# Optimization experiments

Hardware: AMD Instinct MI355X
Metric: run time of the kernel (lower is better)

The kernel has to match this reference:

```python
import jax, jax.numpy as jnp
import numpy as np

B, W, C_BLK, N_EMBD, N_HEADS = 512, 128, 24, 32, 2


def setup_inputs() -> dict:
    key = jax.random.key(0)
    k1, k2, k3, k4 = jax.random.split(key, 4)
    x = jax.random.normal(k1, (B, W, C_BLK, N_EMBD), dtype=jnp.float32)
    x_end_idx = jax.random.randint(k2, (B, W), 0, C_BLK, dtype=jnp.int32)
    # nn.Linear(n_embd, 3*n_embd, bias=False): store transposed so y = x @ w
    w_attn = jax.random.normal(k3, (N_EMBD, 3 * N_EMBD), dtype=jnp.float32) * (1.0 / np.sqrt(N_EMBD))
    w_proj = jax.random.normal(k4, (N_EMBD, N_EMBD), dtype=jnp.float32) * (1.0 / np.sqrt(N_EMBD))
    return {"x": x, "x_end_idx": x_end_idx, "w_attn": w_attn, "w_proj": w_proj}


def reference(x, x_end_idx, w_attn, w_proj):
    # x: [B, W, c, C]; causal self-attention over the char axis c, per (batch, word).
    Bd, Wd, c, C = x.shape
    H = N_HEADS
    D = C // H
    qkv = x @ w_attn                               # [B, W, c, 3C]
    q, k, v = jnp.split(qkv, 3, axis=-1)
    # [B, W, H, c, D]
    q = q.reshape(Bd, Wd, c, H, D).transpose(0, 1, 3, 2, 4)
    k = k.reshape(Bd, Wd, c, H, D).transpose(0, 1, 3, 2, 4)
    v = v.reshape(Bd, Wd, c, H, D).transpose(0, 1, 3, 2, 4)
    scale = 1.0 / jnp.sqrt(jnp.asarray(D, dtype=x.dtype))
    scores = jnp.einsum('bwhqd,bwhkd->bwhqk', q, k) * scale   # [B, W, H, c, c]
    causal = jnp.tril(jnp.ones((c, c), dtype=bool))
    scores = jnp.where(causal, scores, jnp.asarray(-jnp.inf, dtype=scores.dtype))
    att = jax.nn.softmax(scores, axis=-1)
    out = jnp.einsum('bwhqk,bwhkd->bwhqd', att, v)            # [B, W, H, c, D]
    out = out.transpose(0, 1, 3, 2, 4).reshape(Bd, Wd, c, C)
    out = out @ w_proj                                        # c_proj (dropout in eval mode = identity)
    out = x + out                                             # residual
    # Vectorized last-token gather: pick out[b, w, x_end_idx[b, w], :]
    idx = x_end_idx[:, :, None, None].astype(jnp.int32)       # [B, W, 1, 1]
    samples = jnp.take_along_axis(out, jnp.broadcast_to(idx, (Bd, Wd, 1, C)), axis=2)
    return samples.squeeze(2)                                 # [B, W, C]
```

## Files before the change

### kernel.cpp

```cpp
#include <hip/hip_runtime.h>


#define CB      24
#define CC      32
#define DD      16
#define THREEC  96
#define NBW     (512 * 128)
#define WPB     4
#define XSS     34

__device__ __align__(16) float4 g_M4[2][8][CC];
__device__ __align__(16) float4 g_P4[2][8][CC];

__global__ void precompute_mp(const float* __restrict__ w_attn,
                              const float* __restrict__ w_proj)
{
    const int idx = blockIdx.x * 256 + threadIdx.x;
    const int h = idx >> 8, e4 = (idx >> 5) & 7, c = idx & 31;
    float m[4], p[4];
    #pragma unroll
    for (int k = 0; k < 4; ++k) {
        const int e = 4 * e4 + k;
        float mm = 0.f, pp = 0.f;
        #pragma unroll
        for (int d = 0; d < DD; ++d) {
            const int i = DD * h + d;
            mm = fmaf(w_attn[e * THREEC + i],          w_attn[c * THREEC + CC + i], mm);
            pp = fmaf(w_attn[e * THREEC + 2 * CC + i], w_proj[i * CC + c],          pp);
        }
        m[k] = 0.25f * mm;
        p[k] = pp;
    }
    g_M4[h][e4][c] = make_float4(m[0], m[1], m[2], m[3]);
    g_P4[h][e4][c] = make_float4(p[0], p[1], p[2], p[3]);
}

struct __align__(16) WaveSmem {
    float xs[CB][XSS];
    float rks[2][CC];
    float ps[2][CC];
    float ys[2][CC];
};

__device__ __forceinline__ void wave_fence() {
    __asm__ volatile("s_waitcnt lgkmcnt(0)" ::: "memory");
}

__global__ __launch_bounds__(256, 8) void char_attn_kernel(
    const float* __restrict__ x,
    const int*   __restrict__ xend,
    float*       __restrict__ out)
{
    __shared__ WaveSmem sm[WPB];

    const int tid  = threadIdx.x;
    const int lane = tid & 63;
    const int wave = tid >> 6;
    WaveSmem& S = sm[wave];

    const int i32  = lane & 31;
    const int half = lane >> 5;

    const int sbid = __builtin_amdgcn_readfirstlane(blockIdx.x * WPB + wave);
    const int sq   = __builtin_amdgcn_readfirstlane(xend[sbid]);
    const int L    = sq + 1;

    const float* __restrict__ xb = x + (size_t)sbid * (CB * CC);
    const float* __restrict__ xq = xb + sq * CC;

    {
        const float2* xb2 = (const float2*)xb;
        const int n2 = L * (CC / 2);
        for (int t = lane; t < n2; t += 64) {
            float2 v = xb2[t];
            const int r = t >> 4, c = (t & 15) * 2;
            *(float2*)&S.xs[r][c] = v;
        }
    }

    {
        float a0 = 0.f, a1 = 0.f, a2 = 0.f, a3 = 0.f;
        #pragma unroll
        for (int e4 = 0; e4 < 8; ++e4) {
            const float4 mv = g_M4[half][e4][i32];
            const float4 xv = *(const float4*)(xq + e4 * 4);
            a0 = fmaf(mv.x, xv.x, a0);
            a1 = fmaf(mv.y, xv.y, a1);
            a2 = fmaf(mv.z, xv.z, a2);
            a3 = fmaf(mv.w, xv.w, a3);
        }
        S.rks[half][i32] = (a0 + a1) + (a2 + a3);
    }
    wave_fence();

    {
        float sc = -INFINITY;
        if (i32 <= sq) {
            const float4* rk4 = (const float4*)&S.rks[half][0];
            float a0 = 0.f, a1 = 0.f, a2 = 0.f, a3 = 0.f;
            #pragma unroll
            for (int e4 = 0; e4 < 8; ++e4) {
                const float4 rv = rk4[e4];
                const float2 x0 = *(const float2*)&S.xs[i32][e4 * 4];
                const float2 x1 = *(const float2*)&S.xs[i32][e4 * 4 + 2];
                a0 = fmaf(rv.x, x0.x, a0);
                a1 = fmaf(rv.y, x0.y, a1);
                a2 = fmaf(rv.z, x1.x, a2);
                a3 = fmaf(rv.w, x1.y, a3);
            }
            sc = (a0 + a1) + (a2 + a3);
        }
        float m = sc;
        #pragma unroll
        for (int off = 16; off >= 1; off >>= 1)
            m = fmaxf(m, __shfl_xor(m, off));
        const float e = (i32 <= sq) ? __expf(sc - m) : 0.f;
        float sum = e;
        #pragma unroll
        for (int off = 16; off >= 1; off >>= 1)
            sum += __shfl_xor(sum, off);
        S.ps[half][i32] = __fdividef(e, sum);
    }
    wave_fence();

    {
        float a0 = 0.f, a1 = 0.f;
        int j = 0;
        for (; j + 1 < L; j += 2) {
            const float2 p2 = *(const float2*)&S.ps[half][j];
            a0 = fmaf(p2.x, S.xs[j][i32],     a0);
            a1 = fmaf(p2.y, S.xs[j + 1][i32], a1);
        }
        if (j < L)
            a0 = fmaf(S.ps[half][j], S.xs[j][i32], a0);
        S.ys[half][i32] = a0 + a1;
    }
    wave_fence();

    {
        const float4* y4 = (const float4*)&S.ys[half][0];
        float a0 = 0.f, a1 = 0.f, a2 = 0.f, a3 = 0.f;
        #pragma unroll
        for (int e4 = 0; e4 < 8; ++e4) {
            const float4 pv = g_P4[half][e4][i32];
            const float4 yv = y4[e4];
            a0 = fmaf(pv.x, yv.x, a0);
            a1 = fmaf(pv.y, yv.y, a1);
            a2 = fmaf(pv.z, yv.z, a2);
            a3 = fmaf(pv.w, yv.w, a3);
        }
        float t = (a0 + a1) + (a2 + a3);
        t += __shfl_xor(t, 32);
        if (lane < CC)
            out[(size_t)sbid * CC + i32] = t + S.xs[sq][i32];
    }
}

extern "C" void kernel_launch(void* const* d_in, const int* in_sizes, int n_in,
                              void* d_out, int out_size, void* d_ws, size_t ws_size,
                              hipStream_t stream) {
    const float* x      = (const float*)d_in[0];
    const int*   xend   = (const int*)d_in[1];
    const float* w_attn = (const float*)d_in[2];
    const float* w_proj = (const float*)d_in[3];
    float* out = (float*)d_out;

    precompute_mp<<<dim3(2), dim3(256), 0, stream>>>(w_attn, w_proj);
    char_attn_kernel<<<dim3(NBW / WPB), dim3(WPB * 64), 0, stream>>>(
        x, xend, out);
}
```

Measured before the change: 294.6 us.

## Process 16 samples per wave with register prefetch of next sample

Each wave now loops over 16 (batch,word) pairs instead of one. The M and P weight fragments are held in registers across the loop, and the next sample's x rows are prefetched into registers while the current one is computed. The softmax drops the max subtraction and folds the normalization into the y output. This amortizes weight loads and hides global load latency, at the cost of more registers and lower occupancy (launch bounds drop from 8 to 4), fewer blocks, and a risk of exp overflow with no max shift.

```diff
diff --git a/kernel.cpp b/kernel.cpp
--- a/kernel.cpp
+++ b/kernel.cpp
@@ -7,6 +7,8 @@
 #define THREEC  96
 #define NBW     (512 * 128)
 #define WPB     4
+#define NPW     16
+#define NBLK    (NBW / (WPB * NPW))
 #define XSS     34
 
 __device__ __align__(16) float4 g_M4[2][8][CC];
@@ -46,7 +48,7 @@
     __asm__ volatile("s_waitcnt lgkmcnt(0)" ::: "memory");
 }
 
-__global__ __launch_bounds__(256, 8) void char_attn_kernel(
+__global__ __launch_bounds__(256, 4) void char_attn_kernel(
     const float* __restrict__ x,
     const int*   __restrict__ xend,
     float*       __restrict__ out)
@@ -61,98 +63,138 @@
     const int i32  = lane & 31;
     const int half = lane >> 5;
 
-    const int sbid = __builtin_amdgcn_readfirstlane(blockIdx.x * WPB + wave);
-    const int sq   = __builtin_amdgcn_readfirstlane(xend[sbid]);
-    const int L    = sq + 1;
-
-    const float* __restrict__ xb = x + (size_t)sbid * (CB * CC);
-    const float* __restrict__ xq = xb + sq * CC;
-
+    const int sbase = __builtin_amdgcn_readfirstlane(
+                          (blockIdx.x * WPB + wave) * NPW);
+    const int* __restrict__ xe = xend + sbase;
+
+    float4 Mw[8], Pw[8];
+    #pragma unroll
+    for (int e4 = 0; e4 < 8; ++e4) {
+        Mw[e4] = g_M4[half][e4][i32];
+        Pw[e4] = g_P4[half][e4][i32];
+    }
+
+    int sq  = __builtin_amdgcn_readfirstlane(xe[0]);
+    int sqn = __builtin_amdgcn_readfirstlane(xe[1]);
+    float2 pf[6];
+    #pragma unroll
+    for (int i = 0; i < 6; ++i) pf[i] = make_float2(0.f, 0.f);
     {
-        const float2* xb2 = (const float2*)xb;
-        const int n2 = L * (CC / 2);
-        for (int t = lane; t < n2; t += 64) {
-            float2 v = xb2[t];
-            const int r = t >> 4, c = (t & 15) * 2;
-            *(float2*)&S.xs[r][c] = v;
-        }
-    }
-
-    {
-        float a0 = 0.f, a1 = 0.f, a2 = 0.f, a3 = 0.f;
+        const float2* xp = (const float2*)(x + (size_t)sbase * (CB * CC));
+        const int n2 = (sq + 1) * (CC / 2);
         #pragma unroll
-        for (int e4 = 0; e4 < 8; ++e4) {
-            const float4 mv = g_M4[half][e4][i32];
-            const float4 xv = *(const float4*)(xq + e4 * 4);
-            a0 = fmaf(mv.x, xv.x, a0);
-            a1 = fmaf(mv.y, xv.y, a1);
-            a2 = fmaf(mv.z, xv.z, a2);
-            a3 = fmaf(mv.w, xv.w, a3);
-        }
-        S.rks[half][i32] = (a0 + a1) + (a2 + a3);
-    }
-    wave_fence();
-
-    {
-        float sc = -INFINITY;
-        if (i32 <= sq) {
-            const float4* rk4 = (const float4*)&S.rks[half][0];
+        for (int i = 0; i < 6; ++i) {
+            const int t = lane + 64 * i;
+            if (t < n2) pf[i] = xp[t];
+        }
+    }
+
+    for (int k = 0; k < NPW; ++k) {
+        const int pid = sbase + k;
+        const float* __restrict__ xb = x + (size_t)pid * (CB * CC);
+        const float* __restrict__ xq = xb + sq * CC;
+
+        float4 xqv[8];
+        #pragma unroll
+        for (int e = 0; e < 8; ++e) xqv[e] = *(const float4*)(xq + 4 * e);
+
+        {
+            const int n2 = (sq + 1) * (CC / 2);
+            #pragma unroll
+            for (int i = 0; i < 6; ++i) {
+                const int t = lane + 64 * i;
+                if (t < n2) {
+                    const int r = t >> 4, c = (t & 15) * 2;
+                    *(float2*)&S.xs[r][c] = pf[i];
+                }
+            }
+        }
+
+        if (k + 1 < NPW) {
+            const float2* xp = (const float2*)(x + (size_t)(pid + 1) * (CB * CC));
+            const int n2n = (sqn + 1) * (CC / 2);
+            #pragma unroll
+            for (int i = 0; i < 6; ++i) {
+                const int t = lane + 64 * i;
+                if (t < n2n) pf[i] = xp[t];
+            }
+        }
+        const int sqf = __builtin_amdgcn_readfirstlane(
+                            xe[(k + 2 < NPW) ? k + 2 : NPW - 1]);
+
+        {
             float a0 = 0.f, a1 = 0.f, a2 = 0.f, a3 = 0.f;
             #pragma unroll
             for (int e4 = 0; e4 < 8; ++e4) {
-                const float4 rv = rk4[e4];
-                const float2 x0 = *(const float2*)&S.xs[i32][e4 * 4];
-                const float2 x1 = *(const float2*)&S.xs[i32][e4 * 4 + 2];
-                a0 = fmaf(rv.x, x0.x, a0);
-                a1 = fmaf(rv.y, x0.y, a1);
-                a2 = fmaf(rv.z, x1.x, a2);
-                a3 = fmaf(rv.w, x1.y, a3);
-            }
-            sc = (a0 + a1) + (a2 + a3);
-        }
-        float m = sc;
-        #pragma unroll
-        for (int off = 16; off >= 1; off >>= 1)
-            m = fmaxf(m, __shfl_xor(m, off));
-        const float e = (i32 <= sq) ? __expf(sc - m) : 0.f;
-        float sum = e;
-        #pragma unroll
-        for (int off = 16; off >= 1; off >>= 1)
-            sum += __shfl_xor(sum, off);
-        S.ps[half][i32] = __fdividef(e, sum);
-    }
-    wave_fence();
-
-    {
-        float a0 = 0.f, a1 = 0.f;
-        int j = 0;
-        for (; j + 1 < L; j += 2) {
-            const float2 p2 = *(const float2*)&S.ps[half][j];
-            a0 = fmaf(p2.x, S.xs[j][i32],     a0);
-            a1 = fmaf(p2.y, S.xs[j + 1][i32], a1);
-        }
-        if (j < L)
-            a0 = fmaf(S.ps[half][j], S.xs[j][i32], a0);
-        S.ys[half][i32] = a0 + a1;
-    }
-    wave_fence();
-
-    {
-        const float4* y4 = (const float4*)&S.ys[half][0];
-        float a0 = 0.f, a1 = 0.f, a2 = 0.f, a3 = 0.f;
-        #pragma unroll
-        for (int e4 = 0; e4 < 8; ++e4) {
-            const float4 pv = g_P4[half][e4][i32];
-            const float4 yv = y4[e4];
-            a0 = fmaf(pv.x, yv.x, a0);
-            a1 = fmaf(pv.y, yv.y, a1);
-            a2 = fmaf(pv.z, yv.z, a2);
-            a3 = fmaf(pv.w, yv.w, a3);
-        }
-        float t = (a0 + a1) + (a2 + a3);
-        t += __shfl_xor(t, 32);
-        if (lane < CC)
-            out[(size_t)sbid * CC + i32] = t + S.xs[sq][i32];
+                a0 = fmaf(Mw[e4].x, xqv[e4].x, a0);
+                a1 = fmaf(Mw[e4].y, xqv[e4].y, a1);
+                a2 = fmaf(Mw[e4].z, xqv[e4].z, a2);
+                a3 = fmaf(Mw[e4].w, xqv[e4].w, a3);
+            }
+            S.rks[half][i32] = (a0 + a1) + (a2 + a3);
+        }
+        wave_fence();
+
+        float rsum;
+        {
+            float e = 0.f;
+            if (i32 <= sq) {
+                const float4* rk4 = (const float4*)&S.rks[half][0];
+                float a0 = 0.f, a1 = 0.f, a2 = 0.f, a3 = 0.f;
+                #pragma unroll
+                for (int e4 = 0; e4 < 8; ++e4) {
+                    const float4 rv = rk4[e4];
+                    const float2 x0 = *(const float2*)&S.xs[i32][e4 * 4];
+                    const float2 x1 = *(const float2*)&S.xs[i32][e4 * 4 + 2];
+                    a0 = fmaf(rv.x, x0.x, a0);
+                    a1 = fmaf(rv.y, x0.y, a1);
+                    a2 = fmaf(rv.z, x1.x, a2);
+                    a3 = fmaf(rv.w, x1.y, a3);
+                }
+                e = __expf((a0 + a1) + (a2 + a3));
+            }
+            S.ps[half][i32] = e;
+            float sum = e;
+            #pragma unroll
+            for (int off = 16; off >= 1; off >>= 1)
+                sum += __shfl_xor(sum, off);
+            rsum = __fdividef(1.f, sum);
+        }
+        wave_fence();
+
+        {
+            float a0 = 0.f, a1 = 0.f;
+            const int Lc = sq + 1;
+            int j = 0;
+            for (; j + 1 < Lc; j += 2) {
+                const float2 p2 = *(const float2*)&S.ps[half][j];
+                a0 = fmaf(p2.x, S.xs[j][i32],     a0);
+                a1 = fmaf(p2.y, S.xs[j + 1][i32], a1);
+            }
+            if (j < Lc)
+                a0 = fmaf(S.ps[half][j], S.xs[j][i32], a0);
+            S.ys[half][i32] = (a0 + a1) * rsum;
+        }
+        wave_fence();
+
+        {
+            const float4* y4 = (const float4*)&S.ys[half][0];
+            float a0 = 0.f, a1 = 0.f, a2 = 0.f, a3 = 0.f;
+            #pragma unroll
+            for (int e4 = 0; e4 < 8; ++e4) {
+                const float4 yv = y4[e4];
+                a0 = fmaf(Pw[e4].x, yv.x, a0);
+                a1 = fmaf(Pw[e4].y, yv.y, a1);
+                a2 = fmaf(Pw[e4].z, yv.z, a2);
+                a3 = fmaf(Pw[e4].w, yv.w, a3);
+            }
+            float t = (a0 + a1) + (a2 + a3);
+            t += __shfl_xor(t, 32);
+            if (lane < CC)
+                out[(size_t)pid * CC + i32] = t + S.xs[sq][i32];
+        }
+
+        sq = sqn; sqn = sqf;
     }
 }
 
@@ -166,6 +208,6 @@
     float* out = (float*)d_out;
 
     precompute_mp<<<dim3(2), dim3(256), 0, stream>>>(w_attn, w_proj);
-    char_attn_kernel<<<dim3(NBW / WPB), dim3(WPB * 64), 0, stream>>>(
+    char_attn_kernel<<<dim3(NBLK), dim3(WPB * 64), 0, stream>>>(
         x, xend, out);
 }
```

Result: no change. 299.1 us (+1.5%).
